# Kernel tuning notes

Measured on AMD Instinct MI355X. Metric: run time of the kernel, lower is better.

Reference implementation:

```python
import jax, jax.numpy as jnp
import numpy as np

D = 256; H = 8; L = 4; P = 4; DFF = 2048; DH = D // H
SPATIAL_SHAPES = [(96, 96), (48, 48), (24, 24), (12, 12)]
S = sum(h * w for h, w in SPATIAL_SHAPES)  # 12240
NQ = 900; B = 8


def layer_norm(x, g, b, eps=1e-5):
    m = x.mean(-1, keepdims=True)
    v = ((x - m) ** 2).mean(-1, keepdims=True)
    return (x - m) * jax.lax.rsqrt(v + eps) * g + b


def mha(q, k, v, in_w, in_b, out_w, out_b):
    # torch nn.MultiheadAttention, seq-first (Q,B,D)
    Wq, Wk, Wv = jnp.split(in_w, 3, axis=0)
    bq, bk, bv = jnp.split(in_b, 3, axis=0)
    def proj(x, W, b):
        y = x @ W.T + b
        return y.reshape(x.shape[0], x.shape[1], H, DH).transpose(1, 2, 0, 3)  # (B,H,Q,DH)
    qh, kh, vh = proj(q, Wq, bq), proj(k, Wk, bk), proj(v, Wv, bv)
    scores = jnp.einsum('bhqd,bhkd->bhqk', qh, kh) * np.float32(1.0 / np.sqrt(DH))
    attn = jax.nn.softmax(scores, axis=-1)
    o = jnp.einsum('bhqk,bhkd->bhqd', attn, vh)
    o = o.transpose(2, 0, 1, 3).reshape(q.shape[0], q.shape[1], D)
    return o @ out_w.T + out_b


def bilinear_sample(value_lvl, loc, h, w):
    # value_lvl: (B,H,h*w,DH); loc: (B,Q,H,P,2) normalized in [0,1]
    # grid_sample semantics: align_corners=False, zero padding
    x = loc[..., 0] * w - 0.5
    y = loc[..., 1] * h - 0.5
    x0 = jnp.floor(x); y0 = jnp.floor(y)
    lx = x - x0; ly = y - y0
    x0i = x0.astype(jnp.int32); y0i = y0.astype(jnp.int32)
    def corner(xi, yi, wgt):
        valid = (xi >= 0) & (xi < w) & (yi >= 0) & (yi < h)
        idx = jnp.clip(yi, 0, h - 1) * w + jnp.clip(xi, 0, w - 1)  # (B,Q,H,P)
        idxT = idx.transpose(0, 2, 1, 3)  # (B,H,Q,P)
        b_, q_ = idxT.shape[0], idxT.shape[2]
        g = jnp.take_along_axis(value_lvl, idxT.reshape(b_, H, -1, 1), axis=2)
        g = g.reshape(b_, H, q_, P, DH)
        wv = (wgt * valid).transpose(0, 2, 1, 3)[..., None]  # (B,H,Q,P,1)
        return g * wv
    return (corner(x0i, y0i, (1 - lx) * (1 - ly)) + corner(x0i + 1, y0i, lx * (1 - ly))
            + corner(x0i, y0i + 1, (1 - lx) * ly) + corner(x0i + 1, y0i + 1, lx * ly))


def deform_attn(q_in, ref, memory_bt, pad_mask, off_w, off_b, aw_w, aw_b, val_w, val_b, out_w, out_b):
    # q_in: (B,Q,D); ref: (B,Q,4); memory_bt: (B,S,D)
    b, q, _ = q_in.shape
    value = memory_bt @ val_w.T + val_b
    value = jnp.where(pad_mask[:, :, None], 0.0, value)
    value = value.reshape(b, S, H, DH).transpose(0, 2, 1, 3)  # (B,H,S,DH)
    offs = (q_in @ off_w.T + off_b).reshape(b, q, H, L, P, 2)
    w = jax.nn.softmax((q_in @ aw_w.T + aw_b).reshape(b, q, H, L * P), axis=-1).reshape(b, q, H, L, P)
    ref_xy = ref[:, :, None, None, None, :2]
    ref_wh = ref[:, :, None, None, None, 2:]
    loc = ref_xy + offs / P * ref_wh * 0.5  # (B,Q,H,L,P,2)
    start = 0
    sampled = []
    for lvl, (hh, ww) in enumerate(SPATIAL_SHAPES):
        sampled.append(bilinear_sample(value[:, :, start:start + hh * ww], loc[:, :, :, lvl], hh, ww))
        start += hh * ww
    samp = jnp.stack(sampled, axis=3)  # (B,H,Q,L,P,DH)
    wT = w.transpose(0, 2, 1, 3, 4)    # (B,H,Q,L,P)
    out = (samp * wT[..., None]).sum(axis=(3, 4))  # (B,H,Q,DH)
    out = out.transpose(0, 2, 1, 3).reshape(b, q, D)
    return out @ out_w.T + out_b


def setup_inputs() -> dict:
    key = jax.random.key(0)
    ks = jax.random.split(key, 16)
    sc = 0.02
    inp = {
        'queries': jax.random.normal(ks[0], (NQ, B, D), jnp.float32),
        'query_position_embeddings': jax.random.normal(ks[1], (NQ, B, D), jnp.float32),
        'query_reference_points': jax.random.uniform(ks[2], (NQ, B, 4), jnp.float32),
        'memory': jax.random.normal(ks[3], (S, B, D), jnp.float32),
        'memory_key_padding_mask': jnp.zeros((B, S), jnp.bool_),
        'memory_level_start_index': jnp.array([0] + list(np.cumsum([h * w for h, w in SPATIAL_SHAPES])[:-1]), jnp.int32),
        'memory_spatial_shapes': jnp.array(SPATIAL_SHAPES, jnp.int32),
        'in_proj_w': jax.random.normal(ks[4], (3 * D, D), jnp.float32) * sc,
        'in_proj_b': jnp.zeros((3 * D,), jnp.float32),
        'out_proj_w': jax.random.normal(ks[5], (D, D), jnp.float32) * sc,
        'out_proj_b': jnp.zeros((D,), jnp.float32),
        'norm1_g': jnp.ones((D,), jnp.float32), 'norm1_b': jnp.zeros((D,), jnp.float32),
        'norm2_g': jnp.ones((D,), jnp.float32), 'norm2_b': jnp.zeros((D,), jnp.float32),
        'norm3_g': jnp.ones((D,), jnp.float32), 'norm3_b': jnp.zeros((D,), jnp.float32),
        'lin1_w': jax.random.normal(ks[6], (DFF, D), jnp.float32) * sc,
        'lin1_b': jnp.zeros((DFF,), jnp.float32),
        'lin2_w': jax.random.normal(ks[7], (D, DFF), jnp.float32) * sc,
        'lin2_b': jnp.zeros((D,), jnp.float32),
        'off_w': jax.random.normal(ks[8], (H * L * P * 2, D), jnp.float32) * sc,
        'off_b': jax.random.normal(ks[9], (H * L * P * 2,), jnp.float32) * 0.5,
        'aw_w': jax.random.normal(ks[10], (H * L * P, D), jnp.float32) * sc,
        'aw_b': jnp.zeros((H * L * P,), jnp.float32),
        'val_w': jax.random.normal(ks[11], (D, D), jnp.float32) * sc,
        'val_b': jnp.zeros((D,), jnp.float32),
        'cout_w': jax.random.normal(ks[12], (D, D), jnp.float32) * sc,
        'cout_b': jnp.zeros((D,), jnp.float32),
    }
    return inp


def reference(queries, query_position_embeddings, query_reference_points, memory,
              memory_key_padding_mask, memory_level_start_index, memory_spatial_shapes,
              in_proj_w, in_proj_b, out_proj_w, out_proj_b,
              norm1_g, norm1_b, norm2_g, norm2_b, norm3_g, norm3_b,
              lin1_w, lin1_b, lin2_w, lin2_b,
              off_w, off_b, aw_w, aw_b, val_w, val_b, cout_w, cout_b):
    # ---- self-attention (dropout = identity, eval mode) ----
    qk = queries + query_position_embeddings
    sa = mha(qk, qk, queries, in_proj_w, in_proj_b, out_proj_w, out_proj_b)
    queries = layer_norm(queries + sa, norm2_g, norm2_b)
    # ---- deformable cross-attention ----
    q_in = (queries + query_position_embeddings).transpose(1, 0, 2)  # (B,Q,D)
    ref = query_reference_points.transpose(1, 0, 2)                  # (B,Q,4)
    mem = memory.transpose(1, 0, 2)                                  # (B,S,D)
    ca = deform_attn(q_in, ref, mem, memory_key_padding_mask,
                     off_w, off_b, aw_w, aw_b, val_w, val_b, cout_w, cout_b)
    queries = layer_norm(queries + ca.transpose(1, 0, 2), norm1_g, norm1_b)
    # ---- FFN ----
    ffn = jax.nn.relu(queries @ lin1_w.T + lin1_b) @ lin2_w.T + lin2_b
    queries = layer_norm(queries + ffn, norm3_g, norm3_b)
    return queries
```

## Files before the change

kernel.cpp:

```cpp
#include <hip/hip_runtime.h>
#include <hip/hip_bf16.h>

#define D_DIM 256
#define H_HEADS 8
#define L_LVLS 4
#define P_PTS 4
#define DFF 2048
#define DH 32
#define NQ 900
#define B_BATCH 8
#define S_TOT 12240
#define NROW (NQ * B_BATCH)
#define KPAD 928

typedef __attribute__((ext_vector_type(8))) short short8;
typedef __attribute__((ext_vector_type(4))) short short4v;
typedef __attribute__((ext_vector_type(4))) float f32x4;

__device__ __forceinline__ short f2bf(float x) {
  union { float f; unsigned u; } v; v.f = x;
  unsigned r = v.u + 0x7fff + ((v.u >> 16) & 1);
  return (short)(r >> 16);
}
__device__ __forceinline__ float bf2f(unsigned short u) {
  union { unsigned u; float f; } v; v.u = ((unsigned)u) << 16; return v.f;
}

#define NB_ADD 1800
struct WConvArgs {
  const float* src[8];
  short* dst[8];
  int end[8];
  int total;
};
__global__ __launch_bounds__(256) void prep_kernel(
    WConvArgs a, const float* __restrict__ q, const float* __restrict__ p,
    short* __restrict__ qk_bf, short* __restrict__ q_bf) {
  if (blockIdx.x < NB_ADD) {
    int t = blockIdx.x * 256 + threadIdx.x;
    float4 x = ((const float4*)q)[t];
    float4 y = ((const float4*)p)[t];
    short4v s, ad;
    s.x = f2bf(x.x); s.y = f2bf(x.y); s.z = f2bf(x.z); s.w = f2bf(x.w);
    ad.x = f2bf(x.x + y.x); ad.y = f2bf(x.y + y.y);
    ad.z = f2bf(x.z + y.z); ad.w = f2bf(x.w + y.w);
    ((short4v*)q_bf)[t] = s;
    ((short4v*)qk_bf)[t] = ad;
  } else {
    int i = (blockIdx.x - NB_ADD) * 256 + threadIdx.x;
    if (i >= a.total) return;
    int seg = 0;
    while (seg < 7 && i >= a.end[seg]) seg++;
    int base = seg ? a.end[seg - 1] : 0;
    a.dst[seg][i - base] = f2bf(a.src[seg][i - base]);
  }
}

template<bool RELU, int OMODE, int TM>
__global__ __launch_bounds__(256) void gemm_bf16(
    const short* __restrict__ A, const short* __restrict__ W,
    const float* __restrict__ bias, void* __restrict__ Cv,
    int M, int N, int K, int LDC) {
  constexpr int MI = (TM == 128) ? 4 : 2;
  __shared__ short As[TM * 40];
  __shared__ short Bs[128 * 40];
  int tid = threadIdx.x;
  int wave = tid >> 6, lane = tid & 63;
  int wm = wave >> 1, wn = wave & 1;
  int quad = lane >> 4, l16 = lane & 15;
  int m0 = blockIdx.y * TM, n0 = blockIdx.x * 128;
  int srowB = tid >> 1, shalfB = tid & 1;
  const short* bsrc = W + (long)(n0 + srowB) * K + shalfB * 16;
  short* bdst = &Bs[srowB * 40 + shalfB * 16];
  const short* asrc; short* adst; bool avalid;
  if (TM == 128) {
    int srow = tid >> 1, shalf = tid & 1;
    int am = m0 + srow;
    avalid = am < M;
    asrc = A + (long)(avalid ? am : 0) * K + shalf * 16;
    adst = &As[srow * 40 + shalf * 16];
  } else {
    int srow = tid >> 2, spart = tid & 3;
    int am = m0 + srow;
    avalid = am < M;
    asrc = A + (long)(avalid ? am : 0) * K + spart * 8;
    adst = &As[srow * 40 + spart * 8];
  }
  f32x4 acc[MI][4] = {};
  short8 ta0 = {}, ta1 = {}, tb0, tb1;
  if (avalid) {
    ta0 = *(const short8*)(asrc);
    if (TM == 128) ta1 = *(const short8*)(asrc + 8);
  }
  tb0 = *(const short8*)(bsrc);
  tb1 = *(const short8*)(bsrc + 8);
  for (int k0 = 0; k0 < K; k0 += 32) {
    __syncthreads();
    *(short8*)adst = ta0;
    if (TM == 128) *(short8*)(adst + 8) = ta1;
    *(short8*)bdst = tb0;
    *(short8*)(bdst + 8) = tb1;
    __syncthreads();
    int kn = k0 + 32;
    if (kn < K) {
      if (avalid) {
        ta0 = *(const short8*)(asrc + kn);
        if (TM == 128) ta1 = *(const short8*)(asrc + kn + 8);
      }
      tb0 = *(const short8*)(bsrc + kn);
      tb1 = *(const short8*)(bsrc + kn + 8);
    }
    short8 af[MI], bf[4];
    #pragma unroll
    for (int i = 0; i < MI; i++)
      af[i] = *(const short8*)&As[(wm * (TM / 2) + i * 16 + l16) * 40 + quad * 8];
    #pragma unroll
    for (int j = 0; j < 4; j++)
      bf[j] = *(const short8*)&Bs[(wn * 64 + j * 16 + l16) * 40 + quad * 8];
    #pragma unroll
    for (int i = 0; i < MI; i++)
      #pragma unroll
      for (int j = 0; j < 4; j++)
        acc[i][j] = __builtin_amdgcn_mfma_f32_16x16x32_bf16(af[i], bf[j], acc[i][j], 0, 0, 0);
  }
  #pragma unroll
  for (int i = 0; i < MI; i++) {
    int mbase = m0 + wm * (TM / 2) + i * 16 + quad * 4;
    #pragma unroll
    for (int r = 0; r < 4; r++) {
      int m = mbase + r;
      if (m < M) {
        #pragma unroll
        for (int j = 0; j < 4; j++) {
          int n = n0 + wn * 64 + j * 16 + l16;
          float v = acc[i][j][r] + bias[n];
          if (RELU) v = fmaxf(v, 0.f);
          if (OMODE == 0) {
            ((float*)Cv)[(long)m * LDC + n] = v;
          } else if (OMODE == 1) {
            ((short*)Cv)[(long)m * LDC + n] = f2bf(v);
          } else if (OMODE == 2) {
            int nq = m >> 3, bb = m & 7;
            int buf = n >> 8, hh = (n >> 5) & 7, dd = n & 31;
            if (buf == 0) v *= 0.25503483f;
            ((short*)Cv)[((long)(buf * 64 + bb * 8 + hh) * KPAD + nq) * 32 + dd] = f2bf(v);
          } else {
            int nq = m >> 3, bb = m & 7;
            int hh = n >> 5, dd = n & 31;
            ((short*)Cv)[((long)(bb * 8 + hh) * 32 + dd) * KPAD + nq] = f2bf(v);
          }
        }
      }
    }
  }
}

__global__ __launch_bounds__(256) void gemm_val(
    const float* __restrict__ A, const short* __restrict__ W,
    const float* __restrict__ bias, short* __restrict__ C) {
  __shared__ short As[128 * 40];
  __shared__ short Bs[128 * 40];
  int tid = threadIdx.x;
  int wave = tid >> 6, lane = tid & 63;
  int wm = wave >> 1, wn = wave & 1;
  int quad = lane >> 4, l16 = lane & 15;
  int m0 = blockIdx.y * 128, n0 = blockIdx.x * 128;
  int srow = tid >> 1, shalf = tid & 1;
  int am = m0 + srow;
  int b = am / S_TOT, s = am - b * S_TOT;
  const float* asrc = A + ((long)s * B_BATCH + b) * 256 + shalf * 16;
  const short* bsrc = W + (long)(n0 + srow) * 256 + shalf * 16;
  short* adst = &As[srow * 40 + shalf * 16];
  short* bdst = &Bs[srow * 40 + shalf * 16];
  f32x4 acc[4][4] = {};
  float4 f0 = ((const float4*)asrc)[0];
  float4 f1 = ((const float4*)asrc)[1];
  float4 f2 = ((const float4*)asrc)[2];
  float4 f3 = ((const float4*)asrc)[3];
  short8 tb0 = *(const short8*)(bsrc);
  short8 tb1 = *(const short8*)(bsrc + 8);
  for (int k0 = 0; k0 < 256; k0 += 32) {
    short8 ta0, ta1;
    ta0[0]=f2bf(f0.x); ta0[1]=f2bf(f0.y); ta0[2]=f2bf(f0.z); ta0[3]=f2bf(f0.w);
    ta0[4]=f2bf(f1.x); ta0[5]=f2bf(f1.y); ta0[6]=f2bf(f1.z); ta0[7]=f2bf(f1.w);
    ta1[0]=f2bf(f2.x); ta1[1]=f2bf(f2.y); ta1[2]=f2bf(f2.z); ta1[3]=f2bf(f2.w);
    ta1[4]=f2bf(f3.x); ta1[5]=f2bf(f3.y); ta1[6]=f2bf(f3.z); ta1[7]=f2bf(f3.w);
    __syncthreads();
    *(short8*)adst = ta0;
    *(short8*)(adst + 8) = ta1;
    *(short8*)bdst = tb0;
    *(short8*)(bdst + 8) = tb1;
    __syncthreads();
    int kn = k0 + 32;
    if (kn < 256) {
      f0 = ((const float4*)(asrc + kn))[0];
      f1 = ((const float4*)(asrc + kn))[1];
      f2 = ((const float4*)(asrc + kn))[2];
      f3 = ((const float4*)(asrc + kn))[3];
      tb0 = *(const short8*)(bsrc + kn);
      tb1 = *(const short8*)(bsrc + kn + 8);
    }
    short8 af[4], bf[4];
    #pragma unroll
    for (int i = 0; i < 4; i++) {
      af[i] = *(const short8*)&As[(wm * 64 + i * 16 + l16) * 40 + quad * 8];
      bf[i] = *(const short8*)&Bs[(wn * 64 + i * 16 + l16) * 40 + quad * 8];
    }
    #pragma unroll
    for (int i = 0; i < 4; i++)
      #pragma unroll
      for (int j = 0; j < 4; j++)
        acc[i][j] = __builtin_amdgcn_mfma_f32_16x16x32_bf16(af[i], bf[j], acc[i][j], 0, 0, 0);
  }
  #pragma unroll
  for (int i = 0; i < 4; i++) {
    int mbase = m0 + wm * 64 + i * 16 + quad * 4;
    #pragma unroll
    for (int r = 0; r < 4; r++) {
      int m = mbase + r;
      #pragma unroll
      for (int j = 0; j < 4; j++) {
        int n = n0 + wn * 64 + j * 16 + l16;
        C[(long)m * 256 + n] = f2bf(acc[i][j][r] + bias[n]);
      }
    }
  }
}

__global__ __launch_bounds__(256) void attn_mfma(
    const short* __restrict__ qk_h, const short* __restrict__ vT,
    short* __restrict__ att) {
  int bh = blockIdx.y; int b = bh >> 3, h = bh & 7;
  int tid = threadIdx.x; int wave = tid >> 6, lane = tid & 63;
  int quad = lane >> 4, l16 = lane & 15;
  int q0 = blockIdx.x * 128 + wave * 32;
  const short* qb = qk_h + (long)bh * KPAD * 32;
  const short* kb = qk_h + (long)(64 + bh) * KPAD * 32;
  const short* vb = vT + (long)bh * 32 * KPAD;
  __shared__ short P[4][32][40];
  short8 qfr[2];
  #pragma unroll
  for (int i = 0; i < 2; i++) {
    int qrow = q0 + i * 16 + l16; if (qrow > 927) qrow = 927;
    qfr[i] = *(const short8*)(qb + (long)qrow * 32 + quad * 8);
  }
  f32x4 acc[2][2] = {};
  float lsum[2] = {0.f, 0.f};
  const f32x4 zero = {0.f, 0.f, 0.f, 0.f};
  short8 ka = *(const short8*)(kb + (long)l16 * 32 + quad * 8);
  short8 kc = *(const short8*)(kb + (long)(16 + l16) * 32 + quad * 8);
  short8 va = *(const short8*)(vb + (long)l16 * KPAD + quad * 8);
  short8 vc = *(const short8*)(vb + (long)(16 + l16) * KPAD + quad * 8);
  for (int t = 0; t < 29; t++) {
    int k0 = t * 32;
    int kn = (t < 28) ? k0 + 32 : k0;
    short8 nka = *(const short8*)(kb + (long)(kn + l16) * 32 + quad * 8);
    short8 nkc = *(const short8*)(kb + (long)(kn + 16 + l16) * 32 + quad * 8);
    short8 nva = *(const short8*)(vb + (long)l16 * KPAD + kn + quad * 8);
    short8 nvc = *(const short8*)(vb + (long)(16 + l16) * KPAD + kn + quad * 8);
    f32x4 s[2][2];
    s[0][0] = __builtin_amdgcn_mfma_f32_16x16x32_bf16(ka, qfr[0], zero, 0, 0, 0);
    s[0][1] = __builtin_amdgcn_mfma_f32_16x16x32_bf16(ka, qfr[1], zero, 0, 0, 0);
    s[1][0] = __builtin_amdgcn_mfma_f32_16x16x32_bf16(kc, qfr[0], zero, 0, 0, 0);
    s[1][1] = __builtin_amdgcn_mfma_f32_16x16x32_bf16(kc, qfr[1], zero, 0, 0, 0);
    float p[2][2][4];
    #pragma unroll
    for (int kf = 0; kf < 2; kf++)
      #pragma unroll
      for (int qf = 0; qf < 2; qf++)
        #pragma unroll
        for (int r = 0; r < 4; r++) {
          float pe = __builtin_amdgcn_exp2f(s[kf][qf][r]);
          if (t == 28) {
            int kid = k0 + kf * 16 + quad * 4 + r;
            if (kid >= 900) pe = 0.f;
          }
          p[kf][qf][r] = pe;
          lsum[qf] += pe;
        }
    #pragma unroll
    for (int kf = 0; kf < 2; kf++)
      #pragma unroll
      for (int qf = 0; qf < 2; qf++)
        #pragma unroll
        for (int r = 0; r < 4; r += 2) {
          unsigned ua = __float_as_uint(p[kf][qf][r]) + 0x7fffu;
          unsigned ub = __float_as_uint(p[kf][qf][r + 1]) + 0x7fffu;
          unsigned pk = (ua >> 16) | (ub & 0xffff0000u);
          *(unsigned*)&P[wave][qf * 16 + l16][kf * 16 + quad * 4 + r] = pk;
        }
    #pragma unroll
    for (int qf = 0; qf < 2; qf++) {
      short8 pf = *(const short8*)&P[wave][qf * 16 + l16][quad * 8];
      acc[0][qf] = __builtin_amdgcn_mfma_f32_16x16x32_bf16(va, pf, acc[0][qf], 0, 0, 0);
      acc[1][qf] = __builtin_amdgcn_mfma_f32_16x16x32_bf16(vc, pf, acc[1][qf], 0, 0, 0);
    }
    ka = nka; kc = nkc; va = nva; vc = nvc;
  }
  #pragma unroll
  for (int qf = 0; qf < 2; qf++) {
    lsum[qf] += __shfl_xor(lsum[qf], 16);
    lsum[qf] += __shfl_xor(lsum[qf], 32);
  }
  #pragma unroll
  for (int df = 0; df < 2; df++)
    #pragma unroll
    for (int qf = 0; qf < 2; qf++) {
      int qg = q0 + qf * 16 + l16;
      if (qg < 900) {
        float inv = 1.f / lsum[qf];
        int d0 = df * 16 + quad * 4;
        short4v o4;
        o4.x = f2bf(acc[df][qf][0] * inv);
        o4.y = f2bf(acc[df][qf][1] * inv);
        o4.z = f2bf(acc[df][qf][2] * inv);
        o4.w = f2bf(acc[df][qf][3] * inv);
        *(short4v*)(att + (long)(qg * 8 + b) * 256 + h * 32 + d0) = o4;
      }
    }
}

template<int BMODE>
__global__ __launch_bounds__(256) void resid_ln(
    const float* __restrict__ X, const float* __restrict__ R,
    const float* __restrict__ g, const float* __restrict__ be,
    float* __restrict__ out, short* __restrict__ obf,
    const float* __restrict__ qpe, short* __restrict__ obft) {
  int row = blockIdx.x;
  int d = threadIdx.x;
  long rrow;
  if (BMODE == 0) rrow = row;
  else { int b = row % B_BATCH; int n = row / B_BATCH; rrow = (long)b * NQ + n; }
  float x = X[(long)row * 256 + d] + R[rrow * 256 + d];
  float s1 = x, s2 = x * x;
  #pragma unroll
  for (int off = 32; off; off >>= 1) {
    s1 += __shfl_xor(s1, off);
    s2 += __shfl_xor(s2, off);
  }
  __shared__ float a1[4], a2[4];
  int w = d >> 6, lidx = d & 63;
  if (lidx == 0) { a1[w] = s1; a2[w] = s2; }
  __syncthreads();
  float S1 = a1[0] + a1[1] + a1[2] + a1[3];
  float S2 = a2[0] + a2[1] + a2[2] + a2[3];
  float mean = S1 * (1.f / 256.f);
  float var = S2 * (1.f / 256.f) - mean * mean;
  float y = (x - mean) * rsqrtf(var + 1e-5f) * g[d] + be[d];
  out[(long)row * 256 + d] = y;
  if (obf) obf[(long)row * 256 + d] = f2bf(y);
  if (obft) {
    int n = row >> 3, b = row & 7;
    obft[((long)b * NQ + n) * 256 + d] = f2bf(y + qpe[(long)row * 256 + d]);
  }
}

__global__ __launch_bounds__(256) void deform_sample(
    const unsigned short* __restrict__ value, const float* __restrict__ offs,
    const float* __restrict__ aw, const float* __restrict__ qrp,
    short* __restrict__ samp) {
  int bq = blockIdx.x;
  int b = bq / NQ, q = bq % NQ;
  int h = threadIdx.x >> 5, c = threadIdx.x & 31;
  __shared__ float Wl[8][16], Lx[8][16], Ly[8][16];
  if (c < 16) {
    float a = aw[(long)bq * 384 + h * 16 + c];
    float ox = offs[(long)bq * 384 + (h * 16 + c) * 2 + 0];
    float oy = offs[(long)bq * 384 + (h * 16 + c) * 2 + 1];
    const float* rp = qrp + ((long)q * B_BATCH + b) * 4;
    Lx[h][c] = rp[0] + ox * 0.25f * rp[2] * 0.5f;
    Ly[h][c] = rp[1] + oy * 0.25f * rp[3] * 0.5f;
    Wl[h][c] = a;
  }
  __syncthreads();
  if (threadIdx.x < 8) {
    int hh = threadIdx.x;
    float mx = -1e30f;
    for (int i = 0; i < 16; i++) mx = fmaxf(mx, Wl[hh][i]);
    float sm = 0.f;
    for (int i = 0; i < 16; i++) { float e = __expf(Wl[hh][i] - mx); Wl[hh][i] = e; sm += e; }
    float inv = 1.f / sm;
    for (int i = 0; i < 16; i++) Wl[hh][i] *= inv;
  }
  __syncthreads();
  const int lvlW[4] = {96, 48, 24, 12};
  const int lvlS[4] = {0, 9216, 11520, 12096};
  float acc = 0.f;
  const unsigned short* vb = value + (long)b * S_TOT * 256 + h * 32 + c;
  #pragma unroll
  for (int l = 0; l < 4; l++) {
    int ww = lvlW[l], hh2 = lvlW[l], st = lvlS[l];
    #pragma unroll
    for (int p = 0; p < 4; p++) {
      int lp = l * 4 + p;
      float wgt = Wl[h][lp];
      float x = Lx[h][lp] * ww - 0.5f;
      float y = Ly[h][lp] * hh2 - 0.5f;
      float x0f = floorf(x), y0f = floorf(y);
      float lx = x - x0f, ly = y - y0f;
      int x0 = (int)x0f, y0 = (int)y0f;
      #pragma unroll
      for (int cy = 0; cy < 2; cy++) {
        #pragma unroll
        for (int cx = 0; cx < 2; cx++) {
          int xi = x0 + cx, yi = y0 + cy;
          float cw = (cx ? lx : 1.f - lx) * (cy ? ly : 1.f - ly);
          bool valid = (xi >= 0) && (xi < ww) && (yi >= 0) && (yi < hh2);
          int xc = min(max(xi, 0), ww - 1);
          int yc = min(max(yi, 0), hh2 - 1);
          float vv = bf2f(vb[(long)(st + yc * ww + xc) * 256]);
          acc += (valid ? cw * wgt : 0.f) * vv;
        }
      }
    }
  }
  samp[(long)bq * 256 + h * 32 + c] = f2bf(acc);
}

extern "C" void kernel_launch(void* const* d_in, const int* in_sizes, int n_in,
                              void* d_out, int out_size, void* d_ws, size_t ws_size,
                              hipStream_t stream) {
  const float* queries = (const float*)d_in[0];
  const float* qpe     = (const float*)d_in[1];
  const float* qrp     = (const float*)d_in[2];
  const float* memory  = (const float*)d_in[3];
  const float* in_w    = (const float*)d_in[7];
  const float* in_b    = (const float*)d_in[8];
  const float* out_w   = (const float*)d_in[9];
  const float* out_b   = (const float*)d_in[10];
  const float* n1g = (const float*)d_in[11];
  const float* n1b = (const float*)d_in[12];
  const float* n2g = (const float*)d_in[13];
  const float* n2b = (const float*)d_in[14];
  const float* n3g = (const float*)d_in[15];
  const float* n3b = (const float*)d_in[16];
  const float* l1w = (const float*)d_in[17];
  const float* l1b = (const float*)d_in[18];
  const float* l2w = (const float*)d_in[19];
  const float* l2b = (const float*)d_in[20];
  const float* off_w = (const float*)d_in[21];
  const float* off_b = (const float*)d_in[22];
  const float* aw_w  = (const float*)d_in[23];
  const float* aw_b  = (const float*)d_in[24];
  const float* val_w = (const float*)d_in[25];
  const float* val_b = (const float*)d_in[26];
  const float* cout_w = (const float*)d_in[27];
  const float* cout_b = (const float*)d_in[28];

  float* ws = (float*)d_ws;
  const long E = (long)NROW * 256;
  float* slotA = ws + 0 * E;
  float* slotC = ws + 2 * E;
  float* slotE = ws + 3 * E;
  float* slotF = ws + 4 * E;
  short* bfA = (short*)(ws + 5 * E);
  short* bfB = bfA + E;
  short* bfC = bfB + E;
  short* wbf = bfC + E;
  short* membt = wbf + 1540096;
  short* valbf = membt + 25067520;

  short* qk_h = membt;
  short* vT   = membt + 2L * 64 * KPAD * 32;

  short* w_in   = wbf;
  short* w_out  = w_in + 196608;
  short* w_off  = w_out + 65536;
  short* w_aw   = w_off + 65536;
  short* w_val  = w_aw + 32768;
  short* w_cout = w_val + 65536;
  short* w_l1   = w_cout + 65536;
  short* w_l2   = w_l1 + 524288;
  float* bias_offaw = (float*)(valbf + 25067520);

  dim3 blk(256);
  dim3 g7200(NROW);

  WConvArgs wa;
  wa.src[0] = in_w;  wa.dst[0] = w_in;
  wa.src[1] = out_w; wa.dst[1] = w_out;
  wa.src[2] = off_w; wa.dst[2] = w_off;
  wa.src[3] = aw_w;  wa.dst[3] = w_aw;
  wa.src[4] = val_w; wa.dst[4] = w_val;
  wa.src[5] = cout_w;wa.dst[5] = w_cout;
  wa.src[6] = l1w;   wa.dst[6] = w_l1;
  wa.src[7] = l2w;   wa.dst[7] = w_l2;
  int cs[8] = {196608, 65536, 65536, 32768, 65536, 65536, 524288, 524288};
  int acc0 = 0;
  for (int i = 0; i < 8; i++) { acc0 += cs[i]; wa.end[i] = acc0; }
  wa.total = acc0;
  int nbw = (acc0 + 255) / 256;
  prep_kernel<<<dim3(NB_ADD + nbw), blk, 0, stream>>>(wa, queries, qpe, bfA, bfB);
  hipMemcpyAsync(bias_offaw, off_b, 256 * sizeof(float), hipMemcpyDeviceToDevice, stream);
  hipMemcpyAsync(bias_offaw + 256, aw_b, 128 * sizeof(float), hipMemcpyDeviceToDevice, stream);

  gemm_bf16<false, 2, 128><<<dim3(4, 57), blk, 0, stream>>>(bfA, w_in, in_b, qk_h, NROW, 512, 256, 512);
  gemm_bf16<false, 3, 64><<<dim3(2, 113), blk, 0, stream>>>(bfB, w_in + 131072, in_b + 512, vT, NROW, 256, 256, 256);
  attn_mfma<<<dim3(8, 64), blk, 0, stream>>>(qk_h, vT, bfC);
  gemm_bf16<false, 0, 64><<<dim3(2, 113), blk, 0, stream>>>(bfC, w_out, out_b, slotC, NROW, 256, 256, 256);
  resid_ln<0><<<g7200, blk, 0, stream>>>(queries, slotC, n2g, n2b, slotE, nullptr, qpe, bfB);
  gemm_bf16<false, 0, 64><<<dim3(3, 113), blk, 0, stream>>>(bfB, w_off, bias_offaw, slotA, NROW, 384, 256, 384);
  gemm_val<<<dim3(2, 765), blk, 0, stream>>>(memory, w_val, val_b, valbf);
  deform_sample<<<g7200, blk, 0, stream>>>((const unsigned short*)valbf, slotA, slotA + 256, qrp, bfA);
  gemm_bf16<false, 0, 64><<<dim3(2, 113), blk, 0, stream>>>(bfA, w_cout, cout_b, slotC, NROW, 256, 256, 256);
  resid_ln<1><<<g7200, blk, 0, stream>>>(slotE, slotC, n1g, n1b, slotF, bfC, nullptr, nullptr);
  gemm_bf16<true, 1, 128><<<dim3(16, 57), blk, 0, stream>>>(bfC, w_l1, l1b, membt, NROW, DFF, 256, DFF);
  gemm_bf16<false, 0, 64><<<dim3(2, 113), blk, 0, stream>>>(membt, w_l2, l2b, slotC, NROW, 256, 2048, 256);
  resid_ln<0><<<g7200, blk, 0, stream>>>(slotF, slotC, n3g, n3b, (float*)d_out, nullptr, nullptr, nullptr);
}
```

Before: 432.3 us.

## Restructure value-projection GEMM: full-K A tile in LDS, B fragments from global

The value-projection GEMM now loads the whole 64x256 A tile (fp32 memory, converted to bf16) into shared memory once, with a single barrier. The weight fragments are read straight from global into registers with one-step prefetch instead of going through LDS. The M tile drops from 128 to 64 rows, doubling the grid. This removes the per-k-step barriers and LDS traffic for B. In exchange it adds more redundant weight reads from L2 and a larger LDS footprint (about 41KB), which may limit occupancy.

```diff
diff --git a/kernel.cpp b/kernel.cpp
--- a/kernel.cpp
+++ b/kernel.cpp
@@ -155,66 +155,67 @@
   }
 }
 
+#define VCHUNK 2568
 __global__ __launch_bounds__(256) void gemm_val(
     const float* __restrict__ A, const short* __restrict__ W,
     const float* __restrict__ bias, short* __restrict__ C) {
-  __shared__ short As[128 * 40];
-  __shared__ short Bs[128 * 40];
+  __shared__ short As[8 * VCHUNK];
   int tid = threadIdx.x;
   int wave = tid >> 6, lane = tid & 63;
   int wm = wave >> 1, wn = wave & 1;
   int quad = lane >> 4, l16 = lane & 15;
-  int m0 = blockIdx.y * 128, n0 = blockIdx.x * 128;
-  int srow = tid >> 1, shalf = tid & 1;
-  int am = m0 + srow;
-  int b = am / S_TOT, s = am - b * S_TOT;
-  const float* asrc = A + ((long)s * B_BATCH + b) * 256 + shalf * 16;
-  const short* bsrc = W + (long)(n0 + srow) * 256 + shalf * 16;
-  short* adst = &As[srow * 40 + shalf * 16];
-  short* bdst = &Bs[srow * 40 + shalf * 16];
-  f32x4 acc[4][4] = {};
-  float4 f0 = ((const float4*)asrc)[0];
-  float4 f1 = ((const float4*)asrc)[1];
-  float4 f2 = ((const float4*)asrc)[2];
-  float4 f3 = ((const float4*)asrc)[3];
-  short8 tb0 = *(const short8*)(bsrc);
-  short8 tb1 = *(const short8*)(bsrc + 8);
-  for (int k0 = 0; k0 < 256; k0 += 32) {
-    short8 ta0, ta1;
-    ta0[0]=f2bf(f0.x); ta0[1]=f2bf(f0.y); ta0[2]=f2bf(f0.z); ta0[3]=f2bf(f0.w);
-    ta0[4]=f2bf(f1.x); ta0[5]=f2bf(f1.y); ta0[6]=f2bf(f1.z); ta0[7]=f2bf(f1.w);
-    ta1[0]=f2bf(f2.x); ta1[1]=f2bf(f2.y); ta1[2]=f2bf(f2.z); ta1[3]=f2bf(f2.w);
-    ta1[4]=f2bf(f3.x); ta1[5]=f2bf(f3.y); ta1[6]=f2bf(f3.z); ta1[7]=f2bf(f3.w);
-    __syncthreads();
-    *(short8*)adst = ta0;
-    *(short8*)(adst + 8) = ta1;
-    *(short8*)bdst = tb0;
-    *(short8*)(bdst + 8) = tb1;
-    __syncthreads();
-    int kn = k0 + 32;
-    if (kn < 256) {
-      f0 = ((const float4*)(asrc + kn))[0];
-      f1 = ((const float4*)(asrc + kn))[1];
-      f2 = ((const float4*)(asrc + kn))[2];
-      f3 = ((const float4*)(asrc + kn))[3];
-      tb0 = *(const short8*)(bsrc + kn);
-      tb1 = *(const short8*)(bsrc + kn + 8);
-    }
-    short8 af[4], bf[4];
-    #pragma unroll
-    for (int i = 0; i < 4; i++) {
-      af[i] = *(const short8*)&As[(wm * 64 + i * 16 + l16) * 40 + quad * 8];
-      bf[i] = *(const short8*)&Bs[(wn * 64 + i * 16 + l16) * 40 + quad * 8];
-    }
-    #pragma unroll
-    for (int i = 0; i < 4; i++)
+  int m0 = blockIdx.y * 64, n0 = blockIdx.x * 128;
+  {
+    int row = tid >> 2, q = tid & 3;
+    int am = m0 + row;
+    int b = am / S_TOT, s = am - b * S_TOT;
+    const float4* ap = (const float4*)(A + ((long)s * B_BATCH + b) * 256 + q * 64);
+    float4 t[16];
+    #pragma unroll
+    for (int u = 0; u < 16; u++) t[u] = ap[u];
+    #pragma unroll
+    for (int half = 0; half < 2; half++) {
+      short* dst = &As[(2 * q + half) * VCHUNK + row * 40];
+      #pragma unroll
+      for (int u = 0; u < 4; u++) {
+        float4 x = t[half * 8 + 2 * u], y = t[half * 8 + 2 * u + 1];
+        short8 w;
+        w[0] = f2bf(x.x); w[1] = f2bf(x.y); w[2] = f2bf(x.z); w[3] = f2bf(x.w);
+        w[4] = f2bf(y.x); w[5] = f2bf(y.y); w[6] = f2bf(y.z); w[7] = f2bf(y.w);
+        *(short8*)(dst + u * 8) = w;
+      }
+    }
+  }
+  const short* wb[4];
+  #pragma unroll
+  for (int j = 0; j < 4; j++)
+    wb[j] = W + (long)(n0 + wn * 64 + j * 16 + l16) * 256 + quad * 8;
+  short8 bcur[4], bnxt[4];
+  #pragma unroll
+  for (int j = 0; j < 4; j++) bcur[j] = *(const short8*)(wb[j]);
+  f32x4 acc[2][4] = {};
+  __syncthreads();
+  #pragma unroll
+  for (int t = 0; t < 8; t++) {
+    if (t < 7) {
+      #pragma unroll
+      for (int j = 0; j < 4; j++) bnxt[j] = *(const short8*)(wb[j] + (t + 1) * 32);
+    }
+    short8 af[2];
+    #pragma unroll
+    for (int i = 0; i < 2; i++)
+      af[i] = *(const short8*)&As[t * VCHUNK + (wm * 32 + i * 16 + l16) * 40 + quad * 8];
+    #pragma unroll
+    for (int i = 0; i < 2; i++)
       #pragma unroll
       for (int j = 0; j < 4; j++)
-        acc[i][j] = __builtin_amdgcn_mfma_f32_16x16x32_bf16(af[i], bf[j], acc[i][j], 0, 0, 0);
-  }
-  #pragma unroll
-  for (int i = 0; i < 4; i++) {
-    int mbase = m0 + wm * 64 + i * 16 + quad * 4;
+        acc[i][j] = __builtin_amdgcn_mfma_f32_16x16x32_bf16(af[i], bcur[j], acc[i][j], 0, 0, 0);
+    #pragma unroll
+    for (int j = 0; j < 4; j++) bcur[j] = bnxt[j];
+  }
+  #pragma unroll
+  for (int i = 0; i < 2; i++) {
+    int mbase = m0 + wm * 32 + i * 16 + quad * 4;
     #pragma unroll
     for (int r = 0; r < 4; r++) {
       int m = mbase + r;
@@ -500,7 +501,7 @@
   gemm_bf16<false, 0, 64><<<dim3(2, 113), blk, 0, stream>>>(bfC, w_out, out_b, slotC, NROW, 256, 256, 256);
   resid_ln<0><<<g7200, blk, 0, stream>>>(queries, slotC, n2g, n2b, slotE, nullptr, qpe, bfB);
   gemm_bf16<false, 0, 64><<<dim3(3, 113), blk, 0, stream>>>(bfB, w_off, bias_offaw, slotA, NROW, 384, 256, 384);
-  gemm_val<<<dim3(2, 765), blk, 0, stream>>>(memory, w_val, val_b, valbf);
+  gemm_val<<<dim3(2, 1530), blk, 0, stream>>>(memory, w_val, val_b, valbf);
   deform_sample<<<g7200, blk, 0, stream>>>((const unsigned short*)valbf, slotA, slotA + 256, qrp, bfA);
   gemm_bf16<false, 0, 64><<<dim3(2, 113), blk, 0, stream>>>(bfA, w_cout, cout_b, slotC, NROW, 256, 256, 256);
   resid_ln<1><<<g7200, blk, 0, stream>>>(slotE, slotC, n1g, n1b, slotF, bfC, nullptr, nullptr);
```

Measured after the change: 462.0 us. 6.9% more time.
